# Kernel optimization log

Measured on AMD Instinct MI355X. Metric: run time of the kernel, lower is better.

## Reference

```python
import jax, jax.numpy as jnp
import numpy as np

ALPHA = 0.2  # LeakyReLU negative slope
NEG_INF = jnp.float32(-9e15)


def setup_inputs() -> dict:
    key = jax.random.key(0)
    k1, k2, k3, k4, k5, k6 = jax.random.split(key, 6)
    B, N, F_in, F_out = 8, 2048, 256, 64
    h = jax.random.normal(k1, (B, N, F_in), dtype=jnp.float32)
    adj = jax.random.randint(k2, (B, N, N), 0, 2, dtype=jnp.int32)
    level = jax.random.uniform(k3, (B, N), dtype=jnp.float32)
    node_type = jax.random.uniform(k4, (B, N, N), dtype=jnp.float32)
    W = jax.random.normal(k5, (F_in, F_out), dtype=jnp.float32) * 1.414 / np.sqrt(F_in)
    a = jax.random.normal(k6, (2 * F_out, 1), dtype=jnp.float32) * 1.414 / np.sqrt(2 * F_out)
    return {"h": h, "adj": adj, "level": level, "node_type": node_type, "W": W, "a": a}


def reference(h, adj, level, node_type, W, a):
    # h: [B,N,Fin], adj/node_type: [B,N,N], level: [B,N], W: [Fin,Fout], a: [2*Fout,1]
    F_out = W.shape[1]
    Wh = jnp.einsum('bnf,fo->bno', h, W)  # [B,N,Fout]
    # Additive attention decomposed: e[b,i,j] = a1.Wh_i + a2.Wh_j (no O(N^2*2F) tensor)
    a1 = a[:F_out, 0]
    a2 = a[F_out:, 0]
    f1 = Wh @ a1  # [B,N]
    f2 = Wh @ a2  # [B,N]
    e = jax.nn.leaky_relu(f1[:, :, None] + f2[:, None, :], negative_slope=ALPHA)  # [B,N,N]
    # gat_our=True path: node_type scales scores, level scales Wh
    e = e * node_type
    Wh = Wh * level[:, :, None]
    attention = jnp.where(adj > 0, e, NEG_INF)
    attention = jax.nn.softmax(attention, axis=1)  # faithful: original softmax over dim=1
    # dropout p=0 / eval mode -> identity
    h_prime = jnp.einsum('bij,bjo->bio', attention, Wh)  # [B,N,Fout]
    return jax.nn.relu(h_prime)  # concat=True
```

## Files before the change

### kernel.cpp

```cpp
#include <hip/hip_runtime.h>

#define BB 8
#define NN 2048
#define FIN 256
#define FO 64

typedef short short8_t __attribute__((ext_vector_type(8)));
typedef float float4_t __attribute__((ext_vector_type(4)));

__device__ __forceinline__ unsigned short f2bf(float x) {
  unsigned int u = __float_as_uint(x);
  unsigned int r = (u + 0x7fffu + ((u >> 16) & 1u)) >> 16;
  return (unsigned short)r;
}

#define GLD16(gp, lp)                                                          \
  __builtin_amdgcn_global_load_lds(                                            \
      (const __attribute__((address_space(1))) void*)(gp),                     \
      (__attribute__((address_space(3))) void*)(lp), 16, 0, 0)

__global__ __launch_bounds__(256) void k1_gemm(
    const float* __restrict__ h,
    const float* __restrict__ level,
    const float* __restrict__ W,
    const float* __restrict__ a,
    float* __restrict__ V, float* __restrict__ f1, float* __restrict__ f2,
    float* __restrict__ scol)
{
  __shared__ float wlds[128 * 64];
  __shared__ float hs[16 * 260];
  __shared__ float parts1[16 * 17];
  __shared__ float parts2[16 * 17];
  int t = threadIdx.x;
  int b = blockIdx.x >> 7;
  int i0 = (blockIdx.x & 127) * 16;

  if (blockIdx.x < 64) scol[blockIdx.x * 256 + t] = 0.0f;

  {
    int r_ld = t >> 4, f0 = (t & 15) * 16;
    const float* hp = h + (size_t)(b * NN + i0 + r_ld) * FIN + f0;
    float4 x0 = *(const float4*)(hp);
    float4 x1 = *(const float4*)(hp + 4);
    float4 x2 = *(const float4*)(hp + 8);
    float4 x3 = *(const float4*)(hp + 12);
    float* hd = &hs[r_ld * 260 + f0];
    *(float4*)(hd + 0) = x0; *(float4*)(hd + 4) = x1;
    *(float4*)(hd + 8) = x2; *(float4*)(hd + 12) = x3;
  }

  int r = t >> 4;
  int c4 = (t & 15) * 4;
  float4 acc = {0, 0, 0, 0};

  #pragma unroll
  for (int half = 0; half < 2; ++half) {
    __syncthreads();
    #pragma unroll
    for (int q = 0; q < 8; ++q) {
      int idx = q * 1024 + t * 4;
      *(float4*)&wlds[idx] = *(const float4*)&W[half * 8192 + idx];
    }
    __syncthreads();
    for (int f = 0; f < 128; f += 8) {
      float4 hv0 = *(const float4*)&hs[r * 260 + half * 128 + f];
      float4 hv1 = *(const float4*)&hs[r * 260 + half * 128 + f + 4];
      float hvv[8] = {hv0.x, hv0.y, hv0.z, hv0.w, hv1.x, hv1.y, hv1.z, hv1.w};
      #pragma unroll
      for (int k = 0; k < 8; ++k) {
        float4 wv = *(const float4*)&wlds[(f + k) * 64 + c4];
        acc.x += hvv[k] * wv.x; acc.y += hvv[k] * wv.y;
        acc.z += hvv[k] * wv.z; acc.w += hvv[k] * wv.w;
      }
    }
  }

  float p1 = acc.x * a[c4] + acc.y * a[c4 + 1] + acc.z * a[c4 + 2] + acc.w * a[c4 + 3];
  float p2 = acc.x * a[64 + c4] + acc.y * a[64 + c4 + 1] +
             acc.z * a[64 + c4 + 2] + acc.w * a[64 + c4 + 3];
  parts1[r * 17 + (t & 15)] = p1;
  parts2[r * 17 + (t & 15)] = p2;
  __syncthreads();
  if (t < 16) {
    float s1 = 0.f, s2 = 0.f;
    #pragma unroll
    for (int g = 0; g < 16; ++g) { s1 += parts1[t * 17 + g]; s2 += parts2[t * 17 + g]; }
    f1[b * NN + i0 + t] = s1;
    f2[b * NN + i0 + t] = s2;
  }

  float lv = level[b * NN + i0 + r];
  float4 vv = {acc.x * lv, acc.y * lv, acc.z * lv, acc.w * lv};
  *(float4*)&V[(size_t)(b * NN + i0 + r) * FO + c4] = vv;
}

__global__ __launch_bounds__(512) void k2a_stream(
    const int* __restrict__ adj,
    const float* __restrict__ ntp,
    const float* __restrict__ f1,
    const float* __restrict__ f2,
    unsigned short* __restrict__ u_bf,
    float* __restrict__ partials)
{
  int t = threadIdx.x;
  int b = blockIdx.x >> 6;
  int rowblk = blockIdx.x & 63;
  int row0 = rowblk * 32;
  size_t base = (size_t)b * NN;
  int j0 = t * 4;

  float4 f2v = *(const float4*)(f2 + base + j0);
  float acc0 = 0.f, acc1 = 0.f, acc2 = 0.f, acc3 = 0.f;

  size_t rb = (base + row0) * (size_t)NN + j0;
  const int* ap = adj + rb;
  const float* np = ntp + rb;
  unsigned short* up = u_bf + rb;
  const float* f1p = f1 + base + row0;

  #pragma unroll
  for (int g = 0; g < 4; ++g) {
    int4 av[8];
    float4 nv[8];
    #pragma unroll
    for (int rr = 0; rr < 8; ++rr) {
      av[rr] = *(const int4*)(ap + (size_t)(g * 8 + rr) * NN);
      nv[rr] = *(const float4*)(np + (size_t)(g * 8 + rr) * NN);
    }
    #pragma unroll
    for (int rr = 0; rr < 8; ++rr) {
      float f1v = f1p[g * 8 + rr];
      float x0 = f1v + f2v.x; x0 = fmaxf(x0, 0.2f * x0);
      float x1 = f1v + f2v.y; x1 = fmaxf(x1, 0.2f * x1);
      float x2 = f1v + f2v.z; x2 = fmaxf(x2, 0.2f * x2);
      float x3 = f1v + f2v.w; x3 = fmaxf(x3, 0.2f * x3);
      float u0 = (av[rr].x > 0) ? __expf(x0 * nv[rr].x) : 0.0f;
      float u1 = (av[rr].y > 0) ? __expf(x1 * nv[rr].y) : 0.0f;
      float u2 = (av[rr].z > 0) ? __expf(x2 * nv[rr].z) : 0.0f;
      float u3 = (av[rr].w > 0) ? __expf(x3 * nv[rr].w) : 0.0f;
      acc0 += u0; acc1 += u1; acc2 += u2; acc3 += u3;
      unsigned int p0 = (unsigned int)f2bf(u0) | ((unsigned int)f2bf(u1) << 16);
      unsigned int p1 = (unsigned int)f2bf(u2) | ((unsigned int)f2bf(u3) << 16);
      *(uint2*)(up + (size_t)(g * 8 + rr) * NN) = make_uint2(p0, p1);
    }
  }

  *(float4*)(partials + (size_t)(b * 64 + rowblk) * NN + j0) =
      make_float4(acc0, acc1, acc2, acc3);
}

template <int STORE_U>
__global__ __launch_bounds__(512) void k2a_stats(
    const int* __restrict__ adj,
    const float* __restrict__ ntp,
    const float* __restrict__ f1,
    const float* __restrict__ f2,
    unsigned short* __restrict__ u_bf,
    unsigned char* __restrict__ bits,
    float* __restrict__ scol)
{
  __shared__ int ladj[2][16 * 256];
  __shared__ float lnt[2][16 * 256];
  __shared__ float red[2048];
  int t = threadIdx.x;
  int b = blockIdx.x >> 6;
  int row0 = (blockIdx.x & 63) * 32;
  int w = t >> 6, l = t & 63;
  size_t base = (size_t)b * NN;

  auto stage = [&](int buf, int s) {
    int tile = s >> 3, c = s & 7;
    int r0 = row0 + tile * 16 + 2 * w;
    const int* ga = adj + (base + r0) * NN + c * 256 + l * 4;
    const float* gn = ntp + (base + r0) * NN + c * 256 + l * 4;
    GLD16(ga, &ladj[buf][(2 * w) * 256]);
    GLD16(ga + NN, &ladj[buf][(2 * w + 1) * 256]);
    GLD16(gn, &lnt[buf][(2 * w) * 256]);
    GLD16(gn + NN, &lnt[buf][(2 * w + 1) * 256]);
  };

  int jj = t & 255;
  int rh = t >> 8;

  float accJ[8];
  #pragma unroll
  for (int c = 0; c < 8; ++c) accJ[c] = 0.f;
  float f2v[8];
  #pragma unroll
  for (int c = 0; c < 8; ++c) f2v[c] = f2[base + c * 256 + jj];

  stage(0, 0);
  for (int s = 0; s < 16; ++s) {
    int buf = s & 1;
    __syncthreads();
    if (s < 15) stage(buf ^ 1, s + 1);
    int tile = s >> 3, c = s & 7;
    #pragma unroll
    for (int q = 0; q < 8; ++q) {
      int r = rh * 8 + q;
      int av = ladj[buf][r * 256 + jj];
      float nv = lnt[buf][r * 256 + jj];
      float f1v = f1[base + row0 + tile * 16 + r];
      float x = f1v + f2v[c];
      x = fmaxf(x, 0.2f * x);
      bool m = av > 0;
      float u = m ? __expf(x * nv) : 0.0f;
      accJ[c] += u;
      if (STORE_U) {
        u_bf[(base + row0 + tile * 16 + r) * NN + c * 256 + jj] = f2bf(u);
      } else {
        unsigned long long bal = __ballot(m);
        if (l == 0)
          *(unsigned long long*)&bits[(base + row0 + tile * 16 + r) * (NN / 8)
                                      + c * 32 + (w & 3) * 8] = bal;
      }
    }
  }

  if (rh == 0) {
    #pragma unroll
    for (int c = 0; c < 8; ++c) red[c * 256 + jj] = accJ[c];
  }
  __syncthreads();
  if (rh == 1) {
    #pragma unroll
    for (int c = 0; c < 8; ++c) red[c * 256 + jj] += accJ[c];
  }
  __syncthreads();
  #pragma unroll
  for (int q = 0; q < 4; ++q)
    atomicAdd(&scol[base + q * 512 + t], red[q * 512 + t]);
}

__global__ __launch_bounds__(256) void k2b_pack_p(
    const float* __restrict__ V,
    const float* __restrict__ partials,
    unsigned short* __restrict__ vf)
{
  __shared__ float sred[8 * 32];
  __shared__ float sinv[32];
  int t = threadIdx.x;
  int b = blockIdx.x >> 6;
  int kk = blockIdx.x & 63;

  {
    int tj = t & 31, tr = t >> 5;
    float s = 0.f;
    #pragma unroll
    for (int q = 0; q < 8; ++q)
      s += partials[(size_t)(b * 64 + tr * 8 + q) * NN + kk * 32 + tj];
    sred[tr * 32 + tj] = s;
  }
  __syncthreads();
  if (t < 32) {
    float tot = 0.f;
    #pragma unroll
    for (int g = 0; g < 8; ++g) tot += sred[g * 32 + t];
    sinv[t] = (tot > 0.f) ? (1.0f / tot) : 0.0f;
  }
  __syncthreads();

  int ng = t >> 6;
  int l = t & 63;
  int jb0 = (l >> 4) * 8;
  int jb = kk * 32 + jb0;
  int o = ng * 16 + (l & 15);
  unsigned int pk[4];
  #pragma unroll
  for (int p = 0; p < 4; ++p) {
    int jr0 = jb + 2 * p, jr1 = jb + 2 * p + 1;
    float i0 = sinv[jb0 + 2 * p];
    float i1 = sinv[jb0 + 2 * p + 1];
    float v0 = V[(size_t)(b * NN + jr0) * FO + o] * i0;
    float v1 = V[(size_t)(b * NN + jr1) * FO + o] * i1;
    pk[p] = (unsigned int)f2bf(v0) | ((unsigned int)f2bf(v1) << 16);
  }
  *(uint4*)(vf + (size_t)(((b * 64 + kk) * 4 + ng) * 64 + l) * 8) =
      make_uint4(pk[0], pk[1], pk[2], pk[3]);
}

__global__ __launch_bounds__(256) void k2b_pack(
    const float* __restrict__ V,
    const float* __restrict__ scol,
    unsigned short* __restrict__ vf)
{
  int t = threadIdx.x;
  int b = blockIdx.x >> 6;
  int kk = blockIdx.x & 63;
  int ng = t >> 6;
  int l = t & 63;
  int jb = kk * 32 + ((l >> 4) * 8);
  int o = ng * 16 + (l & 15);
  unsigned int pk[4];
  #pragma unroll
  for (int p = 0; p < 4; ++p) {
    int jr0 = jb + 2 * p, jr1 = jb + 2 * p + 1;
    float s0 = scol[b * NN + jr0];
    float s1 = scol[b * NN + jr1];
    float i0 = (s0 > 0.f) ? (1.0f / s0) : 0.0f;
    float i1 = (s1 > 0.f) ? (1.0f / s1) : 0.0f;
    float v0 = V[(size_t)(b * NN + jr0) * FO + o] * i0;
    float v1 = V[(size_t)(b * NN + jr1) * FO + o] * i1;
    pk[p] = (unsigned int)f2bf(v0) | ((unsigned int)f2bf(v1) << 16);
  }
  *(uint4*)(vf + (size_t)(((b * 64 + kk) * 4 + ng) * 64 + l) * 8) =
      make_uint4(pk[0], pk[1], pk[2], pk[3]);
}

__global__ __launch_bounds__(512, 4) void k3_agg_u3(
    const unsigned short* __restrict__ u_bf,
    const unsigned short* __restrict__ vf,
    float* __restrict__ outp)
{
  __shared__ float red[8 * 16 * 68];
  int t = threadIdx.x;
  int b = blockIdx.x >> 6;
  int tt = blockIdx.x & 63;
  int i0 = tt * 32;
  int w = t >> 6, l = t & 63;
  int col = l & 15, quad = l >> 4;
  const unsigned short* urow0 = u_bf + (size_t)(b * NN + i0 + col) * NN + quad * 8;
  const unsigned short* urow1 = urow0 + (size_t)16 * NN;
  const unsigned short* vbase = vf + (size_t)(b * 64) * 2048 + l * 8;

  float4_t acc[2][4];
  #pragma unroll
  for (int sgi = 0; sgi < 2; ++sgi)
    #pragma unroll
    for (int g = 0; g < 4; ++g) acc[sgi][g] = (float4_t){0, 0, 0, 0};

  int kk0 = w * 8;
  short8_t A0 = *(const short8_t*)(urow0 + kk0 * 32);
  short8_t A1 = *(const short8_t*)(urow1 + kk0 * 32);
  const unsigned short* vb0 = vbase + (size_t)kk0 * 2048;
  short8_t c0 = *(const short8_t*)(vb0);
  short8_t c1 = *(const short8_t*)(vb0 + 512);
  short8_t c2 = *(const short8_t*)(vb0 + 1024);
  short8_t c3 = *(const short8_t*)(vb0 + 1536);

  #pragma unroll
  for (int s = 0; s < 8; ++s) {
    short8_t nA0, nA1, n0, n1, n2, n3;
    if (s < 7) {
      int kk = w * 8 + s + 1;
      nA0 = *(const short8_t*)(urow0 + kk * 32);
      nA1 = *(const short8_t*)(urow1 + kk * 32);
      const unsigned short* vn = vbase + (size_t)kk * 2048;
      n0 = *(const short8_t*)(vn);
      n1 = *(const short8_t*)(vn + 512);
      n2 = *(const short8_t*)(vn + 1024);
      n3 = *(const short8_t*)(vn + 1536);
    }
    acc[0][0] = __builtin_amdgcn_mfma_f32_16x16x32_bf16(A0, c0, acc[0][0], 0, 0, 0);
    acc[0][1] = __builtin_amdgcn_mfma_f32_16x16x32_bf16(A0, c1, acc[0][1], 0, 0, 0);
    acc[0][2] = __builtin_amdgcn_mfma_f32_16x16x32_bf16(A0, c2, acc[0][2], 0, 0, 0);
    acc[0][3] = __builtin_amdgcn_mfma_f32_16x16x32_bf16(A0, c3, acc[0][3], 0, 0, 0);
    acc[1][0] = __builtin_amdgcn_mfma_f32_16x16x32_bf16(A1, c0, acc[1][0], 0, 0, 0);
    acc[1][1] = __builtin_amdgcn_mfma_f32_16x16x32_bf16(A1, c1, acc[1][1], 0, 0, 0);
    acc[1][2] = __builtin_amdgcn_mfma_f32_16x16x32_bf16(A1, c2, acc[1][2], 0, 0, 0);
    acc[1][3] = __builtin_amdgcn_mfma_f32_16x16x32_bf16(A1, c3, acc[1][3], 0, 0, 0);
    if (s < 7) { A0 = nA0; A1 = nA1; c0 = n0; c1 = n1; c2 = n2; c3 = n3; }
  }

  #pragma unroll
  for (int sub = 0; sub < 2; ++sub) {
    __syncthreads();
    #pragma unroll
    for (int r = 0; r < 4; ++r) {
      int rowi = quad * 4 + r;
      float* rp = &red[w * 1088 + rowi * 68 + col];
      rp[0] = acc[sub][0][r];
      rp[16] = acc[sub][1][r];
      rp[32] = acc[sub][2][r];
      rp[48] = acc[sub][3][r];
    }
    __syncthreads();
    if (t < 256) {
      int row = t >> 4, o4 = (t & 15) * 4;
      const float* rp = &red[row * 68 + o4];
      float4 s0 = *(const float4*)(rp);
      float4 s1 = *(const float4*)(rp + 1088);
      float4 s2 = *(const float4*)(rp + 2176);
      float4 s3 = *(const float4*)(rp + 3264);
      float4 s4 = *(const float4*)(rp + 4352);
      float4 s5 = *(const float4*)(rp + 5440);
      float4 s6 = *(const float4*)(rp + 6528);
      float4 s7 = *(const float4*)(rp + 7616);
      float4 o;
      o.x = fmaxf(s0.x + s1.x + s2.x + s3.x + s4.x + s5.x + s6.x + s7.x, 0.0f);
      o.y = fmaxf(s0.y + s1.y + s2.y + s3.y + s4.y + s5.y + s6.y + s7.y, 0.0f);
      o.z = fmaxf(s0.z + s1.z + s2.z + s3.z + s4.z + s5.z + s6.z + s7.z, 0.0f);
      o.w = fmaxf(s0.w + s1.w + s2.w + s3.w + s4.w + s5.w + s6.w + s7.w, 0.0f);
      *(float4*)&outp[(size_t)(b * NN + i0 + sub * 16 + row) * FO + o4] = o;
    }
  }
}

__global__ __launch_bounds__(256) void k3_agg_b(
    const float* __restrict__ ntp,
    const unsigned char* __restrict__ bits,
    const float* __restrict__ f1,
    const float* __restrict__ f2,
    const unsigned short* __restrict__ vf,
    float* __restrict__ outp)
{
  __shared__ float red[4 * 16 * 68];
  int t = threadIdx.x;
  int b = blockIdx.x >> 7;
  int i0 = (blockIdx.x & 127) * 16;
  int w = t >> 6, l = t & 63;
  int col = l & 15, quad = l >> 4;
  int gi = b * NN + i0 + col;
  float f1v = f1[gi];
  const float* ntrow = ntp + (size_t)gi * NN;
  const unsigned char* brow = bits + (size_t)gi * (NN / 8);
  float4_t acc0 = {0, 0, 0, 0}, acc1 = {0, 0, 0, 0}, acc2 = {0, 0, 0, 0}, acc3 = {0, 0, 0, 0};

  for (int s = 0; s < 16; ++s) {
    int kk = w * 16 + s;
    int jq = kk * 32 + quad * 8;
    unsigned int m8 = brow[jq >> 3];
    float4 n0 = *(const float4*)(ntrow + jq);
    float4 n1 = *(const float4*)(ntrow + jq + 4);
    float4 g0 = *(const float4*)(f2 + b * NN + jq);
    float4 g1 = *(const float4*)(f2 + b * NN + jq + 4);
    float f2v[8] = {g0.x, g0.y, g0.z, g0.w, g1.x, g1.y, g1.z, g1.w};
    float ntf[8] = {n0.x, n0.y, n0.z, n0.w, n1.x, n1.y, n1.z, n1.w};
    union { unsigned int u[4]; short8_t v; } A;
    #pragma unroll
    for (int p = 0; p < 4; ++p) {
      int e0 = 2 * p, e1 = 2 * p + 1;
      float x0 = f1v + f2v[e0]; x0 = fmaxf(x0, 0.2f * x0);
      float u0 = ((m8 >> e0) & 1u) ? __expf(x0 * ntf[e0]) : 0.0f;
      float x1 = f1v + f2v[e1]; x1 = fmaxf(x1, 0.2f * x1);
      float u1 = ((m8 >> e1) & 1u) ? __expf(x1 * ntf[e1]) : 0.0f;
      A.u[p] = (unsigned int)f2bf(u0) | ((unsigned int)f2bf(u1) << 16);
    }
    const unsigned short* vb = vf + (size_t)(b * 64 + kk) * 2048 + l * 8;
    short8_t bf0 = *(const short8_t*)(vb);
    short8_t bf1 = *(const short8_t*)(vb + 512);
    short8_t bf2 = *(const short8_t*)(vb + 1024);
    short8_t bf3 = *(const short8_t*)(vb + 1536);
    acc0 = __builtin_amdgcn_mfma_f32_16x16x32_bf16(A.v, bf0, acc0, 0, 0, 0);
    acc1 = __builtin_amdgcn_mfma_f32_16x16x32_bf16(A.v, bf1, acc1, 0, 0, 0);
    acc2 = __builtin_amdgcn_mfma_f32_16x16x32_bf16(A.v, bf2, acc2, 0, 0, 0);
    acc3 = __builtin_amdgcn_mfma_f32_16x16x32_bf16(A.v, bf3, acc3, 0, 0, 0);
  }

  #pragma unroll
  for (int r = 0; r < 4; ++r) {
    int rowi = quad * 4 + r;
    red[w * 1088 + rowi * 68 + 0 + col] = acc0[r];
    red[w * 1088 + rowi * 68 + 16 + col] = acc1[r];
    red[w * 1088 + rowi * 68 + 32 + col] = acc2[r];
    red[w * 1088 + rowi * 68 + 48 + col] = acc3[r];
  }
  __syncthreads();

  int row = t >> 4, o4 = (t & 15) * 4;
  const float* rp = &red[row * 68 + o4];
  float4 s0 = *(const float4*)(rp);
  float4 s1 = *(const float4*)(rp + 1088);
  float4 s2 = *(const float4*)(rp + 2176);
  float4 s3 = *(const float4*)(rp + 3264);
  float4 o;
  o.x = fmaxf(s0.x + s1.x + s2.x + s3.x, 0.0f);
  o.y = fmaxf(s0.y + s1.y + s2.y + s3.y, 0.0f);
  o.z = fmaxf(s0.z + s1.z + s2.z + s3.z, 0.0f);
  o.w = fmaxf(s0.w + s1.w + s2.w + s3.w, 0.0f);
  *(float4*)&outp[(size_t)(b * NN + i0 + row) * FO + o4] = o;
}

extern "C" void kernel_launch(void* const* d_in, const int* in_sizes, int n_in,
                              void* d_out, int out_size, void* d_ws, size_t ws_size,
                              hipStream_t stream) {
  const float* h = (const float*)d_in[0];
  const int* adj = (const int*)d_in[1];
  const float* level = (const float*)d_in[2];
  const float* ntm = (const float*)d_in[3];
  const float* W = (const float*)d_in[4];
  const float* a = (const float*)d_in[5];
  float* outp = (float*)d_out;

  float* V = (float*)d_ws;
  float* f1 = V + (size_t)BB * NN * FO;
  float* f2 = f1 + BB * NN;
  float* scol = f2 + BB * NN;
  unsigned short* vf = (unsigned short*)(scol + BB * NN);
  float* partials = (float*)(vf + (size_t)BB * NN * FO);
  char* tail = (char*)(partials + (size_t)BB * 64 * NN);
  size_t fixed = (size_t)(tail - (char*)d_ws);
  size_t need_u = fixed + (size_t)BB * NN * NN * 2;
  bool big = (ws_size >= need_u);

  k1_gemm<<<1024, 256, 0, stream>>>(h, level, W, a, V, f1, f2, scol);
  if (big) {
    unsigned short* u_bf = (unsigned short*)tail;
    k2a_stream<<<512, 512, 0, stream>>>(adj, ntm, f1, f2, u_bf, partials);
    k2b_pack_p<<<512, 256, 0, stream>>>(V, partials, vf);
    k3_agg_u3<<<512, 512, 0, stream>>>(u_bf, vf, outp);
  } else {
    unsigned char* bits = (unsigned char*)tail;
    k2a_stats<0><<<512, 512, 0, stream>>>(adj, ntm, f1, f2, nullptr, bits, scol);
    k2b_pack<<<512, 256, 0, stream>>>(V, scol, vf);
    k3_agg_b<<<1024, 256, 0, stream>>>(ntm, bits, f1, f2, vf, outp);
  }
}
```

Measured before the change: 339.6 us.

## Precompute adjacency bitmask in separate pass before streaming softmax kernel

Adds a k0_bits pre-pass that reads the int32 adjacency with nontemporal loads and packs it into a 1-bit-per-entry mask. The streaming exp kernel then loads a small bitmask tile into LDS instead of reading adj alongside node_type. The intent is to split the two large input streams so each kernel has simpler access patterns and less register pressure. In exchange it adds a kernel launch, a few MB of extra mask traffic and more workspace. The old adj-reading path is kept as a fallback when the workspace is too small.

```diff
diff --git a/kernel.cpp b/kernel.cpp
--- a/kernel.cpp
+++ b/kernel.cpp
@@ -7,6 +7,7 @@
 
 typedef short short8_t __attribute__((ext_vector_type(8)));
 typedef float float4_t __attribute__((ext_vector_type(4)));
+typedef int int4_v __attribute__((ext_vector_type(4)));
 
 __device__ __forceinline__ unsigned short f2bf(float x) {
   unsigned int u = __float_as_uint(x);
@@ -18,6 +19,25 @@
   __builtin_amdgcn_global_load_lds(                                            \
       (const __attribute__((address_space(1))) void*)(gp),                     \
       (__attribute__((address_space(3))) void*)(lp), 16, 0, 0)
+
+__global__ __launch_bounds__(512) void k0_bits(
+    const int* __restrict__ adj, unsigned int* __restrict__ abits)
+{
+  size_t g = (size_t)blockIdx.x * 512 + threadIdx.x;
+  const int4_v* ap = (const int4_v*)adj + g * 8;
+  int4_v a[8];
+  #pragma unroll
+  for (int e = 0; e < 8; ++e) a[e] = __builtin_nontemporal_load(ap + e);
+  unsigned int m = 0;
+  #pragma unroll
+  for (int e = 0; e < 8; ++e) {
+    m |= (a[e].x > 0 ? 1u : 0u) << (4 * e);
+    m |= (a[e].y > 0 ? 1u : 0u) << (4 * e + 1);
+    m |= (a[e].z > 0 ? 1u : 0u) << (4 * e + 2);
+    m |= (a[e].w > 0 ? 1u : 0u) << (4 * e + 3);
+  }
+  abits[g] = m;
+}
 
 __global__ __launch_bounds__(256) void k1_gemm(
     const float* __restrict__ h,
@@ -95,6 +115,70 @@
 }
 
 __global__ __launch_bounds__(512) void k2a_stream(
+    const unsigned int* __restrict__ abits,
+    const float* __restrict__ ntp,
+    const float* __restrict__ f1,
+    const float* __restrict__ f2,
+    unsigned short* __restrict__ u_bf,
+    float* __restrict__ partials)
+{
+  __shared__ unsigned int lbits[32 * 64];
+  __shared__ float sf1[32];
+  int t = threadIdx.x;
+  int b = blockIdx.x >> 6;
+  int rowblk = blockIdx.x & 63;
+  int row0 = rowblk * 32;
+  size_t base = (size_t)b * NN;
+  int j0 = t * 4;
+
+  {
+    const uint4* src = (const uint4*)(abits + (base + row0) * 64);
+    ((uint4*)lbits)[t] = src[t];
+    if (t < 32) sf1[t] = f1[base + row0 + t];
+  }
+
+  float4 f2v = *(const float4*)(f2 + base + j0);
+  float acc0 = 0.f, acc1 = 0.f, acc2 = 0.f, acc3 = 0.f;
+
+  size_t rb = (base + row0) * (size_t)NN + j0;
+  const float* np = ntp + rb;
+  unsigned short* up = u_bf + rb;
+  int wrd = t >> 3;
+  int sh = (t & 7) * 4;
+
+  __syncthreads();
+
+  #pragma unroll
+  for (int g = 0; g < 4; ++g) {
+    float4 nv[8];
+    #pragma unroll
+    for (int rr = 0; rr < 8; ++rr)
+      nv[rr] = *(const float4*)(np + (size_t)(g * 8 + rr) * NN);
+    #pragma unroll
+    for (int rr = 0; rr < 8; ++rr) {
+      int r = g * 8 + rr;
+      unsigned int nib = lbits[r * 64 + wrd] >> sh;
+      float f1v = sf1[r];
+      float x0 = f1v + f2v.x; x0 = fmaxf(x0, 0.2f * x0);
+      float x1 = f1v + f2v.y; x1 = fmaxf(x1, 0.2f * x1);
+      float x2 = f1v + f2v.z; x2 = fmaxf(x2, 0.2f * x2);
+      float x3 = f1v + f2v.w; x3 = fmaxf(x3, 0.2f * x3);
+      float u0 = (nib & 1u) ? __expf(x0 * nv[rr].x) : 0.0f;
+      float u1 = (nib & 2u) ? __expf(x1 * nv[rr].y) : 0.0f;
+      float u2 = (nib & 4u) ? __expf(x2 * nv[rr].z) : 0.0f;
+      float u3 = (nib & 8u) ? __expf(x3 * nv[rr].w) : 0.0f;
+      acc0 += u0; acc1 += u1; acc2 += u2; acc3 += u3;
+      unsigned int p0 = (unsigned int)f2bf(u0) | ((unsigned int)f2bf(u1) << 16);
+      unsigned int p1 = (unsigned int)f2bf(u2) | ((unsigned int)f2bf(u3) << 16);
+      *(uint2*)(up + (size_t)r * NN) = make_uint2(p0, p1);
+    }
+  }
+
+  *(float4*)(partials + (size_t)(b * 64 + rowblk) * NN + j0) =
+      make_float4(acc0, acc1, acc2, acc3);
+}
+
+__global__ __launch_bounds__(512) void k2a_stream_adj(
     const int* __restrict__ adj,
     const float* __restrict__ ntp,
     const float* __restrict__ f1,
@@ -488,19 +572,28 @@
   float* scol = f2 + BB * NN;
   unsigned short* vf = (unsigned short*)(scol + BB * NN);
   float* partials = (float*)(vf + (size_t)BB * NN * FO);
-  char* tail = (char*)(partials + (size_t)BB * 64 * NN);
-  size_t fixed = (size_t)(tail - (char*)d_ws);
-  size_t need_u = fixed + (size_t)BB * NN * NN * 2;
-  bool big = (ws_size >= need_u);
+  unsigned int* abits = (unsigned int*)(partials + (size_t)BB * 64 * NN);
+  char* tail = (char*)(abits + (size_t)BB * NN * (NN / 32));
+  size_t fixed2 = (size_t)(tail - (char*)d_ws);
+  size_t fixed1 = (size_t)((char*)abits - (char*)d_ws);
+  size_t ubytes = (size_t)BB * NN * NN * 2;
+  bool big2 = (ws_size >= fixed2 + ubytes);
+  bool big1 = (ws_size >= fixed1 + ubytes);
 
   k1_gemm<<<1024, 256, 0, stream>>>(h, level, W, a, V, f1, f2, scol);
-  if (big) {
+  if (big2) {
     unsigned short* u_bf = (unsigned short*)tail;
-    k2a_stream<<<512, 512, 0, stream>>>(adj, ntm, f1, f2, u_bf, partials);
+    k0_bits<<<2048, 512, 0, stream>>>(adj, abits);
+    k2a_stream<<<512, 512, 0, stream>>>(abits, ntm, f1, f2, u_bf, partials);
+    k2b_pack_p<<<512, 256, 0, stream>>>(V, partials, vf);
+    k3_agg_u3<<<512, 512, 0, stream>>>(u_bf, vf, outp);
+  } else if (big1) {
+    unsigned short* u_bf = (unsigned short*)abits;
+    k2a_stream_adj<<<512, 512, 0, stream>>>(adj, ntm, f1, f2, u_bf, partials);
     k2b_pack_p<<<512, 256, 0, stream>>>(V, partials, vf);
     k3_agg_u3<<<512, 512, 0, stream>>>(u_bf, vf, outp);
   } else {
-    unsigned char* bits = (unsigned char*)tail;
+    unsigned char* bits = (unsigned char*)abits;
     k2a_stats<0><<<512, 512, 0, stream>>>(adj, ntm, f1, f2, nullptr, bits, scol);
     k2b_pack<<<512, 256, 0, stream>>>(V, scol, vf);
     k3_agg_b<<<1024, 256, 0, stream>>>(ntm, bits, f1, f2, vf, outp);
```

Result: slower. 360.8 us (+6.3%).
